# Kernel optimization log

Measured on AMD Instinct MI355X. Metric: run time of the kernel, lower is better.

The kernel has to match this reference:

```python
import jax, jax.numpy as jnp
import numpy as np

N_HEAD = 8
SPAN = 32
BN_EPS = 1e-5


def setup_inputs() -> dict:
    key = jax.random.key(0)
    k1, k2, k3 = jax.random.split(key, 3)
    d_model = 256
    hc = d_model // N_HEAD
    x = jax.random.normal(k1, (4, d_model, 32, 32, 32), dtype=jnp.float32)
    qkv_weight = jax.random.normal(k2, (2 * d_model, d_model), dtype=jnp.float32) * np.sqrt(1.0 / d_model)
    relative = jax.random.normal(k3, (2 * hc, 2 * SPAN - 1), dtype=jnp.float32) * np.sqrt(1.0 / hc)
    gamma = jnp.ones((2 * d_model,), dtype=jnp.float32)
    beta = jnp.zeros((2 * d_model,), dtype=jnp.float32)
    return {"x": x, "qkv_weight": qkv_weight, "relative": relative, "gamma": gamma, "beta": beta}


def _batchnorm1d_train(x, gamma, beta):
    # x: (N, C, L); training-mode BN with batch statistics (biased var)
    mean = x.mean(axis=(0, 2), keepdims=True)
    var = x.var(axis=(0, 2), keepdims=True)
    return (x - mean) * jax.lax.rsqrt(var + BN_EPS) * gamma[None, :, None] + beta[None, :, None]


def reference(x, qkv_weight, relative, gamma, beta):
    B, C, H, W, T = x.shape
    hc = C // N_HEAD
    # width=False: permute (B,C,H,W,T) -> (B,T,W,C,H); attention along H
    xp = jnp.transpose(x, (0, 4, 3, 1, 2)).reshape(B * T * W, C, H)
    # 1x1 conv == channel matmul: (2C,C) x (N,C,H) -> (N,2C,H)
    qkv = jnp.einsum('oc,ncl->nol', qkv_weight, xp)
    qkv = qkv.reshape(B * T * W, N_HEAD, 2 * hc, H)
    q = qkv[:, :, : hc // 2]          # (N, nh, hc/2, H)
    k = qkv[:, :, hc // 2: hc]        # (N, nh, hc/2, H)
    v = qkv[:, :, hc:]                # (N, nh, hc,   H)
    # relative position table gather: all_emb[c,i,j] = relative[c, i+j]
    idx = jnp.arange(SPAN)[:, None] + jnp.arange(SPAN)[None, :]
    all_emb = relative[:, idx]        # (2hc, span, span)
    q_emb = all_emb[: hc // 2]
    k_emb = all_emb[hc // 2: hc]
    v_emb = all_emb[hc:]
    qr = jnp.einsum('nhci,cij->nhij', q, q_emb)
    kr = jnp.einsum('nhci,cij->nhij', k, k_emb)
    qk = jnp.einsum('nhci,nhcj->nhij', q, k)
    sim = jax.nn.softmax(qk + qr + kr, axis=-1)      # (N, nh, H, H)
    sv = jnp.einsum('nhij,nhcj->nhci', sim, v)       # (N, nh, hc, H)
    sve = jnp.einsum('nhij,cij->nhci', sim, v_emb)   # (N, nh, hc, H)
    # cat along last dim then view (N, 2C, H) == interleave sv/sve per (h,c)
    stacked = jnp.stack([sv, sve], axis=3).reshape(B * T * W, 2 * C, H)
    out = _batchnorm1d_train(stacked, gamma, beta)
    out = out.reshape(B, T, W, C, 2, H).sum(axis=4)  # (B,T,W,C,H)
    return jnp.transpose(out, (0, 3, 4, 2, 1))       # (B,C,H,W,T)
```

## Files before the change

kernel.cpp:

```cpp
#include <hip/hip_runtime.h>
#include <hip/hip_bf16.h>


typedef __attribute__((ext_vector_type(8))) short short8;
typedef __attribute__((ext_vector_type(16))) float f32x16;

__device__ inline unsigned short f2bu(float f) {
  __hip_bfloat16 h = __float2bfloat16(f);
  return *(unsigned short*)&h;
}

#define MFMA32(A, B, C) __builtin_amdgcn_mfma_f32_32x32x16_bf16(A, B, C, 0, 0, 0)

constexpr int S_I = 646;
constexpr int S_C = 10;

__global__ __launch_bounds__(256) void k0_wsplit(
    const float* __restrict__ W, unsigned short* __restrict__ Whi,
    unsigned short* __restrict__ Wlo) {
  const int i = blockIdx.x * 256 + threadIdx.x;
  const float w = W[i];
  const unsigned u = __float_as_uint(w);
  const float fhi = __uint_as_float(u & 0xFFFF0000u);
  const float lo = w - fhi;
  Whi[i] = (unsigned short)(u >> 16);
  Wlo[i] = (unsigned short)(__float_as_uint(lo) >> 16);
}

__global__ __launch_bounds__(256) void k1_mfma(
    const unsigned short* __restrict__ Whi, const unsigned short* __restrict__ Wlo,
    const float* __restrict__ x, __hip_bfloat16* __restrict__ qkv) {
  const int td = threadIdx.x, bx = blockIdx.x;
  const int otile = bx & 3, nt = (bx >> 2) & 255, b = bx >> 10;
  const int w = nt & 31, i0 = (nt >> 5) << 2;
  const int o0 = otile * 128;
  const float* xb = x + (size_t)b * 256 * 32768;

  const int wid = td >> 6, l = td & 63, h = l >> 5, n = l & 31;
  const int wo = wid >> 1, wn = wid & 1;

  const int colsp0 = (i0 + (n >> 3)) * 1024 + w * 32 + (wn * 2) * 8 + (n & 7);
  const float* px0 = xb + colsp0 + (size_t)(h * 8) * 32768;
  const float* px1 = px0 + 8;
  const unsigned short* pwh = Whi + (size_t)(o0 + wo * 64 + n) * 256 + h * 8;
  const unsigned short* pwl = Wlo + (size_t)(o0 + wo * 64 + n) * 256 + h * 8;

  const f32x16 zf = {0, 0, 0, 0, 0, 0, 0, 0, 0, 0, 0, 0, 0, 0, 0, 0};
  f32x16 acc[2][2];
#pragma unroll
  for (int it = 0; it < 2; ++it)
#pragma unroll
    for (int jt = 0; jt < 2; ++jt) acc[it][jt] = zf;

#pragma unroll 4
  for (int kf = 0; kf < 16; ++kf) {
    const float* pk0 = px0 + (size_t)kf * 16 * 32768;
    const float* pk1 = px1 + (size_t)kf * 16 * 32768;
    float xv0[8], xv1[8];
#pragma unroll
    for (int e = 0; e < 8; ++e) {
      xv0[e] = pk0[(size_t)e * 32768];
      xv1[e] = pk1[(size_t)e * 32768];
    }
    short8 ahi[2], alo[2];
#pragma unroll
    for (int it = 0; it < 2; ++it) {
      ahi[it] = *(const short8*)(pwh + it * (32 * 256) + kf * 16);
      alo[it] = *(const short8*)(pwl + it * (32 * 256) + kf * 16);
    }
    short8 bhi0, blo0, bhi1, blo1;
#pragma unroll
    for (int e = 0; e < 8; ++e) {
      const unsigned u0 = __float_as_uint(xv0[e]);
      bhi0[e] = (short)(u0 >> 16);
      blo0[e] = (short)(__float_as_uint(xv0[e] - __uint_as_float(u0 & 0xFFFF0000u)) >> 16);
      const unsigned u1 = __float_as_uint(xv1[e]);
      bhi1[e] = (short)(u1 >> 16);
      blo1[e] = (short)(__float_as_uint(xv1[e] - __uint_as_float(u1 & 0xFFFF0000u)) >> 16);
    }
#pragma unroll
    for (int it = 0; it < 2; ++it) {
      acc[it][0] = MFMA32(ahi[it], bhi0, acc[it][0]);
      acc[it][0] = MFMA32(ahi[it], blo0, acc[it][0]);
      acc[it][0] = MFMA32(alo[it], bhi0, acc[it][0]);
      acc[it][1] = MFMA32(ahi[it], bhi1, acc[it][1]);
      acc[it][1] = MFMA32(ahi[it], blo1, acc[it][1]);
      acc[it][1] = MFMA32(alo[it], bhi1, acc[it][1]);
    }
  }

  __hip_bfloat16* qb2 = qkv + ((size_t)((b * 32 + w) * 8 + otile * 2 + wo)) * 65536 +
                        (size_t)(wn * 2) * 16384 + i0 * 8;
#pragma unroll
  for (int jt = 0; jt < 2; ++jt) {
    __hip_bfloat16* bjt = qb2 + jt * 16384;
#pragma unroll
    for (int it = 0; it < 2; ++it) {
#pragma unroll
      for (int r = 0; r < 16; ++r) {
        const int ch = it * 32 + (r & 3) + 8 * (r >> 2) + 4 * h;
        bjt[ch * 256 + n] = __float2bfloat16(acc[it][jt][r]);
      }
    }
  }
}

__global__ __launch_bounds__(256, 3) void k2_attn_mfma(
    const __hip_bfloat16* __restrict__ qkv, const float* __restrict__ rel,
    unsigned int* __restrict__ stk2, float* __restrict__ stats) {
  __shared__ __align__(16) __hip_bfloat16 slab[20672];
  __shared__ __align__(16) unsigned short Sbuf[4 * 1280];
  __shared__ float statb[4][32][4];

  const int bx = blockIdx.x;
  const int w = bx & 31, head = (bx >> 5) & 7, b = bx >> 8;
  const int td = threadIdx.x;
  const int wid = td >> 6, l = td & 63, h = l >> 5, n = l & 31;

  short8 eqf[2], ekf[2], evf[4];
#pragma unroll
  for (int dt = 0; dt < 2; ++dt)
#pragma unroll
    for (int e = 0; e < 8; ++e) {
      int c = h * 8 + e, d = dt * 32 + n;
      eqf[dt][e] = (d < 63) ? (short)f2bu(rel[c * 63 + d]) : (short)0;
      ekf[dt][e] = (d < 63) ? (short)f2bu(rel[(16 + c) * 63 + d]) : (short)0;
    }
#pragma unroll
  for (int kh = 0; kh < 4; ++kh)
#pragma unroll
    for (int e = 0; e < 8; ++e) {
      int d = kh * 16 + h * 8 + e;
      evf[kh][e] = (d < 63) ? (short)f2bu(rel[(32 + n) * 63 + d]) : (short)0;
    }
  short8 ones;
#pragma unroll
  for (int e = 0; e < 8; ++e) ones[e] = (short)0x3F80;

  const __hip_bfloat16* qbase = qkv + ((size_t)((b * 32 + w) * 8 + head)) * 65536;
  unsigned int* sb = stk2 + ((size_t)((b * 8 + head) * 32 + w)) * 32768;
  unsigned short* Sb = Sbuf + wid * 1280;

  const f32x16 zf = {0, 0, 0, 0, 0, 0, 0, 0, 0, 0, 0, 0, 0, 0, 0, 0};
  float st0 = 0, st1 = 0, st2 = 0, st3 = 0;

  for (int tc = 0; tc < 4; ++tc) {
    const int t0 = tc * 8;
    __syncthreads();
    for (int r = 0; r < 8; ++r) {
      int idx = td + 256 * r;
      const uint4 dat = *(const uint4*)(qbase + (size_t)tc * 16384 + (size_t)idx * 8);
      unsigned int* lp = (unsigned int*)(slab + (idx & 31) * S_I + (idx >> 5) * S_C);
      lp[0] = dat.x; lp[1] = dat.y; lp[2] = dat.z; lp[3] = dat.w;
    }
    __syncthreads();
    for (int u = 0; u < 2; ++u) {
      const int tt = 2 * wid + u;
      const int t = t0 + tt;
      short8 aq, ak;
#pragma unroll
      for (int e = 0; e < 8; ++e) {
        aq[e] = *(const short*)&slab[n * S_I + (h * 8 + e) * S_C + tt];
        ak[e] = *(const short*)&slab[n * S_I + (16 + h * 8 + e) * S_C + tt];
      }
      f32x16 qkD = MFMA32(aq, ak, zf);
      f32x16 Rq0 = MFMA32(aq, eqf[0], zf);
      f32x16 Rq1 = MFMA32(aq, eqf[1], zf);
      f32x16 Rk0 = MFMA32(ak, ekf[0], zf);
      f32x16 Rk1 = MFMA32(ak, ekf[1], zf);
#pragma unroll
      for (int r = 0; r < 16; ++r) {
        int rowr = (r & 3) + 8 * (r >> 2) + 4 * h;
        int d = rowr + n;
        int src = (d & 31) + 32 * h;
        float vq0 = __shfl(Rq0[r], src);
        float vq1 = __shfl(Rq1[r], src);
        float vk0 = __shfl(Rk0[r], src);
        float vk1 = __shfl(Rk1[r], src);
        float s = qkD[r] + (d < 32 ? vq0 + vk0 : vq1 + vk1);
        Sb[rowr * 40 + n] = f2bu(__expf(s));
      }
      short8 bv0, bv1;
#pragma unroll
      for (int e = 0; e < 8; ++e) {
        int j0 = h * 8 + e, j1 = 16 + h * 8 + e;
        bv0[e] = *(const short*)&slab[j0 * S_I + (32 + n) * S_C + tt];
        bv1[e] = *(const short*)&slab[j1 * S_I + (32 + n) * S_C + tt];
      }
      short8 as0 = *(const short8*)(Sb + n * 40 + h * 8);
      short8 as1 = *(const short8*)(Sb + n * 40 + 16 + h * 8);
      f32x16 svD = MFMA32(as1, bv1, MFMA32(as0, bv0, zf));
      f32x16 sumD = MFMA32(as1, ones, MFMA32(as0, ones, zf));
      f32x16 sveD = zf;
#pragma unroll
      for (int kh = 0; kh < 4; ++kh) {
        short8 ap;
#pragma unroll
        for (int e = 0; e < 8; ++e) {
          int k = kh * 16 + h * 8 + e;
          int jj = k - n;
          unsigned short raw = Sb[n * 40 + (jj & 31)];
          ap[e] = ((unsigned)jj < 32u) ? (short)raw : (short)0;
        }
        sveD = MFMA32(ap, evf[kh], sveD);
      }
#pragma unroll
      for (int r = 0; r < 16; ++r) {
        int rowr = (r & 3) + 8 * (r >> 2) + 4 * h;
        float inv = 1.0f / sumD[r];
        float svn = svD[r] * inv, sven = sveD[r] * inv;
        st0 += svn; st1 += svn * svn; st2 += sven; st3 += sven * sven;
        unsigned int pk = (unsigned int)f2bu(svn) | ((unsigned int)f2bu(sven) << 16);
        sb[((size_t)rowr * 32 + t) * 32 + n] = pk;
      }
    }
  }
  st0 += __shfl_xor(st0, 32); st1 += __shfl_xor(st1, 32);
  st2 += __shfl_xor(st2, 32); st3 += __shfl_xor(st3, 32);
  if (h == 0) {
    statb[wid][n][0] = st0; statb[wid][n][1] = st1;
    statb[wid][n][2] = st2; statb[wid][n][3] = st3;
  }
  __syncthreads();
  if (td < 32) {
    float a0 = 0, a1 = 0, a2 = 0, a3 = 0;
    for (int wv = 0; wv < 4; ++wv) {
      a0 += statb[wv][td][0]; a1 += statb[wv][td][1];
      a2 += statb[wv][td][2]; a3 += statb[wv][td][3];
    }
    const int o2 = head * 64 + 2 * td;
    atomicAdd(&stats[o2], a0);
    atomicAdd(&stats[o2 + 1], a2);
    atomicAdd(&stats[512 + o2], a1);
    atomicAdd(&stats[512 + o2 + 1], a3);
  }
}

__global__ __launch_bounds__(256) void k3_finalize2(
    const unsigned int* __restrict__ stk2, const float* __restrict__ stats,
    const float* __restrict__ gamma, const float* __restrict__ beta,
    float* __restrict__ out) {
  __shared__ float trans[4][32][33];
  __shared__ float s_sc[64], s_sh[64];
  const int bx = blockIdx.x;
  const int w = bx & 31, head = (bx >> 5) & 7, b = bx >> 8;
  const int td = threadIdx.x;
  if (td < 64) {
    const int o2 = head * 64 + td;
    const float NINV = 1.f / 131072.f;
    float m = stats[o2] * NINV;
    float v = stats[512 + o2] * NINV - m * m;
    float sc = gamma[o2] * rsqrtf(v + 1e-5f);
    s_sc[td] = sc;
    s_sh[td] = beta[o2] - m * sc;
  }
  __syncthreads();
  const unsigned int* pb = stk2 + ((size_t)((b * 8 + head) * 32 + w)) * 32768;
  float* ob = out + ((size_t)(b * 256 + head * 32)) * 32768 + w * 32;
  const int t = td >> 3, c0 = (td & 7) * 4;
  const int t2 = td & 31, cbase = td >> 5;
  for (int i4 = 0; i4 < 32; i4 += 4) {
#pragma unroll
    for (int m = 0; m < 4; ++m) {
      const uint4 dat = *(const uint4*)(pb + (size_t)(i4 + m) * 1024 + td * 4);
      unsigned int dws[4] = {dat.x, dat.y, dat.z, dat.w};
#pragma unroll
      for (int q = 0; q < 4; ++q) {
        int c = c0 + q;
        float sv = __uint_as_float((dws[q] & 0xFFFFu) << 16);
        float sve = __uint_as_float(dws[q] & 0xFFFF0000u);
        trans[m][c][t] =
            sv * s_sc[2 * c] + sve * s_sc[2 * c + 1] + s_sh[2 * c] + s_sh[2 * c + 1];
      }
    }
    __syncthreads();
#pragma unroll
    for (int m = 0; m < 4; ++m) {
#pragma unroll
      for (int cc = 0; cc < 4; ++cc) {
        int c = cbase + 8 * cc;
        ob[(size_t)c * 32768 + (size_t)(i4 + m) * 1024 + t2] = trans[m][c][t2];
      }
    }
    __syncthreads();
  }
}

extern "C" void kernel_launch(void* const* d_in, const int* in_sizes, int n_in,
                              void* d_out, int out_size, void* d_ws, size_t ws_size,
                              hipStream_t stream) {
  const float* x        = (const float*)d_in[0];
  const float* qkv_w    = (const float*)d_in[1];
  const float* relative = (const float*)d_in[2];
  const float* gamma    = (const float*)d_in[3];
  const float* beta     = (const float*)d_in[4];
  float* out = (float*)d_out;

  __hip_bfloat16* qkv = (__hip_bfloat16*)d_ws;
  unsigned int* stk2 = (unsigned int*)((char*)d_ws + (size_t)134217728);
  float* stats = (float*)((char*)d_ws + (size_t)268435456);
  unsigned short* Whi = (unsigned short*)stk2;
  unsigned short* Wlo = Whi + 131072;

  hipMemsetAsync(stats, 0, 1024 * sizeof(float), stream);
  k0_wsplit<<<dim3(512), dim3(256), 0, stream>>>(qkv_w, Whi, Wlo);
  k1_mfma<<<dim3(4096), dim3(256), 0, stream>>>(Whi, Wlo, x, qkv);
  k2_attn_mfma<<<dim3(1024), dim3(256), 0, stream>>>(qkv, relative, stk2, stats);
  k3_finalize2<<<dim3(1024), dim3(256), 0, stream>>>(stk2, stats, gamma, beta, out);
}
```

Before: 693.2 us.

## Pre-split x into transposed bf16 hi/lo buffers instead of splitting weights

A new pre-pass reads x once, splits each value into bf16 hi/lo parts and writes them channel-contiguous per spatial position into workspace. The GEMM kernel then fetches x operands as 16-byte vector loads instead of strided scalar fp32 loads that it converted in-loop, and instead splits the small weight matrix on the fly. The block order is also changed so consecutive blocks share an output tile. This is meant to cut the uncoalesced strided x reads and in-loop conversion work, at the cost of an extra full read/write pass over x (about 128 MB each way) and per-iteration weight conversion.

```diff
diff --git a/kernel.cpp b/kernel.cpp
--- a/kernel.cpp
+++ b/kernel.cpp
@@ -15,91 +15,106 @@
 constexpr int S_I = 646;
 constexpr int S_C = 10;
 
-__global__ __launch_bounds__(256) void k0_wsplit(
-    const float* __restrict__ W, unsigned short* __restrict__ Whi,
-    unsigned short* __restrict__ Wlo) {
-  const int i = blockIdx.x * 256 + threadIdx.x;
-  const float w = W[i];
-  const unsigned u = __float_as_uint(w);
-  const float fhi = __uint_as_float(u & 0xFFFF0000u);
-  const float lo = w - fhi;
-  Whi[i] = (unsigned short)(u >> 16);
-  Wlo[i] = (unsigned short)(__float_as_uint(lo) >> 16);
+__global__ __launch_bounds__(256) void k0_xsplit(
+    const float* __restrict__ x, unsigned short* __restrict__ xThi,
+    unsigned short* __restrict__ xTlo) {
+  const int bx = blockIdx.x;
+  const int spt = bx & 127, kt = (bx >> 7) & 3, b = bx >> 9;
+  const int sp = spt * 256 + threadIdx.x;
+  const int k0 = kt * 64;
+  const float* xs = x + (size_t)b * 8388608 + (size_t)k0 * 32768 + sp;
+  unsigned int hiw[32], low[32];
+#pragma unroll
+  for (int m = 0; m < 32; ++m) {
+    const float f0 = xs[(size_t)(2 * m) * 32768];
+    const float f1 = xs[(size_t)(2 * m + 1) * 32768];
+    const unsigned u0 = __float_as_uint(f0), u1 = __float_as_uint(f1);
+    const float l0 = f0 - __uint_as_float(u0 & 0xFFFF0000u);
+    const float l1 = f1 - __uint_as_float(u1 & 0xFFFF0000u);
+    hiw[m] = (u0 >> 16) | ((u1 >> 16) << 16);
+    low[m] = (__float_as_uint(l0) >> 16) | ((__float_as_uint(l1) >> 16) << 16);
+  }
+  unsigned short* dh = xThi + (size_t)b * 8388608 + (size_t)sp * 256 + k0;
+  unsigned short* dl = xTlo + (size_t)b * 8388608 + (size_t)sp * 256 + k0;
+#pragma unroll
+  for (int q = 0; q < 8; ++q) {
+    uint4 vh, vl;
+    vh.x = hiw[4 * q]; vh.y = hiw[4 * q + 1]; vh.z = hiw[4 * q + 2]; vh.w = hiw[4 * q + 3];
+    vl.x = low[4 * q]; vl.y = low[4 * q + 1]; vl.z = low[4 * q + 2]; vl.w = low[4 * q + 3];
+    *(uint4*)(dh + 8 * q) = vh;
+    *(uint4*)(dl + 8 * q) = vl;
+  }
 }
 
 __global__ __launch_bounds__(256) void k1_mfma(
-    const unsigned short* __restrict__ Whi, const unsigned short* __restrict__ Wlo,
-    const float* __restrict__ x, __hip_bfloat16* __restrict__ qkv) {
+    const float* __restrict__ Wq, const unsigned short* __restrict__ xThi,
+    const unsigned short* __restrict__ xTlo, __hip_bfloat16* __restrict__ qkv) {
   const int td = threadIdx.x, bx = blockIdx.x;
-  const int otile = bx & 3, nt = (bx >> 2) & 255, b = bx >> 10;
+  const int nt = bx & 255, otile = (bx >> 8) & 3, b = bx >> 10;
   const int w = nt & 31, i0 = (nt >> 5) << 2;
   const int o0 = otile * 128;
-  const float* xb = x + (size_t)b * 256 * 32768;
 
   const int wid = td >> 6, l = td & 63, h = l >> 5, n = l & 31;
   const int wo = wid >> 1, wn = wid & 1;
 
-  const int colsp0 = (i0 + (n >> 3)) * 1024 + w * 32 + (wn * 2) * 8 + (n & 7);
-  const float* px0 = xb + colsp0 + (size_t)(h * 8) * 32768;
-  const float* px1 = px0 + 8;
-  const unsigned short* pwh = Whi + (size_t)(o0 + wo * 64 + n) * 256 + h * 8;
-  const unsigned short* pwl = Wlo + (size_t)(o0 + wo * 64 + n) * 256 + h * 8;
+  const int sp0 = (i0 + (n >> 3)) * 1024 + w * 32 + (wn * 2) * 8 + (n & 7);
+  const unsigned short* pxh = xThi + (size_t)b * 8388608 + (size_t)sp0 * 256 + h * 8;
+  const unsigned short* pxl = xTlo + (size_t)b * 8388608 + (size_t)sp0 * 256 + h * 8;
+  const float* pw = Wq + (size_t)(o0 + wo * 64 + n) * 256 + h * 8;
 
   const f32x16 zf = {0, 0, 0, 0, 0, 0, 0, 0, 0, 0, 0, 0, 0, 0, 0, 0};
-  f32x16 acc[2][2];
-#pragma unroll
-  for (int it = 0; it < 2; ++it)
-#pragma unroll
-    for (int jt = 0; jt < 2; ++jt) acc[it][jt] = zf;
-
-#pragma unroll 4
+  f32x16 acc00 = zf, acc01 = zf, acc10 = zf, acc11 = zf;
+
+#pragma unroll 2
   for (int kf = 0; kf < 16; ++kf) {
-    const float* pk0 = px0 + (size_t)kf * 16 * 32768;
-    const float* pk1 = px1 + (size_t)kf * 16 * 32768;
-    float xv0[8], xv1[8];
+    const int kb = kf * 16;
+    const short8 bhi0 = *(const short8*)(pxh + kb);
+    const short8 blo0 = *(const short8*)(pxl + kb);
+    const short8 bhi1 = *(const short8*)(pxh + 2048 + kb);
+    const short8 blo1 = *(const short8*)(pxl + 2048 + kb);
+    const float4 w0a = *(const float4*)(pw + kb);
+    const float4 w0b = *(const float4*)(pw + kb + 4);
+    const float4 w1a = *(const float4*)(pw + 32 * 256 + kb);
+    const float4 w1b = *(const float4*)(pw + 32 * 256 + kb + 4);
+    float wv0[8] = {w0a.x, w0a.y, w0a.z, w0a.w, w0b.x, w0b.y, w0b.z, w0b.w};
+    float wv1[8] = {w1a.x, w1a.y, w1a.z, w1a.w, w1b.x, w1b.y, w1b.z, w1b.w};
+    short8 ahi0, alo0, ahi1, alo1;
 #pragma unroll
     for (int e = 0; e < 8; ++e) {
-      xv0[e] = pk0[(size_t)e * 32768];
-      xv1[e] = pk1[(size_t)e * 32768];
-    }
-    short8 ahi[2], alo[2];
-#pragma unroll
-    for (int it = 0; it < 2; ++it) {
-      ahi[it] = *(const short8*)(pwh + it * (32 * 256) + kf * 16);
-      alo[it] = *(const short8*)(pwl + it * (32 * 256) + kf * 16);
-    }
-    short8 bhi0, blo0, bhi1, blo1;
-#pragma unroll
-    for (int e = 0; e < 8; ++e) {
-      const unsigned u0 = __float_as_uint(xv0[e]);
-      bhi0[e] = (short)(u0 >> 16);
-      blo0[e] = (short)(__float_as_uint(xv0[e] - __uint_as_float(u0 & 0xFFFF0000u)) >> 16);
-      const unsigned u1 = __float_as_uint(xv1[e]);
-      bhi1[e] = (short)(u1 >> 16);
-      blo1[e] = (short)(__float_as_uint(xv1[e] - __uint_as_float(u1 & 0xFFFF0000u)) >> 16);
-    }
-#pragma unroll
-    for (int it = 0; it < 2; ++it) {
-      acc[it][0] = MFMA32(ahi[it], bhi0, acc[it][0]);
-      acc[it][0] = MFMA32(ahi[it], blo0, acc[it][0]);
-      acc[it][0] = MFMA32(alo[it], bhi0, acc[it][0]);
-      acc[it][1] = MFMA32(ahi[it], bhi1, acc[it][1]);
-      acc[it][1] = MFMA32(ahi[it], blo1, acc[it][1]);
-      acc[it][1] = MFMA32(alo[it], bhi1, acc[it][1]);
-    }
+      const unsigned u0 = __float_as_uint(wv0[e]);
+      ahi0[e] = (short)(u0 >> 16);
+      alo0[e] = (short)(__float_as_uint(wv0[e] - __uint_as_float(u0 & 0xFFFF0000u)) >> 16);
+      const unsigned u1 = __float_as_uint(wv1[e]);
+      ahi1[e] = (short)(u1 >> 16);
+      alo1[e] = (short)(__float_as_uint(wv1[e] - __uint_as_float(u1 & 0xFFFF0000u)) >> 16);
+    }
+    acc00 = MFMA32(ahi0, bhi0, acc00);
+    acc00 = MFMA32(ahi0, blo0, acc00);
+    acc00 = MFMA32(alo0, bhi0, acc00);
+    acc01 = MFMA32(ahi0, bhi1, acc01);
+    acc01 = MFMA32(ahi0, blo1, acc01);
+    acc01 = MFMA32(alo0, bhi1, acc01);
+    acc10 = MFMA32(ahi1, bhi0, acc10);
+    acc10 = MFMA32(ahi1, blo0, acc10);
+    acc10 = MFMA32(alo1, bhi0, acc10);
+    acc11 = MFMA32(ahi1, bhi1, acc11);
+    acc11 = MFMA32(ahi1, blo1, acc11);
+    acc11 = MFMA32(alo1, bhi1, acc11);
   }
 
   __hip_bfloat16* qb2 = qkv + ((size_t)((b * 32 + w) * 8 + otile * 2 + wo)) * 65536 +
                         (size_t)(wn * 2) * 16384 + i0 * 8;
+  const f32x16* accs[2][2] = {{&acc00, &acc01}, {&acc10, &acc11}};
 #pragma unroll
   for (int jt = 0; jt < 2; ++jt) {
     __hip_bfloat16* bjt = qb2 + jt * 16384;
 #pragma unroll
     for (int it = 0; it < 2; ++it) {
+      const f32x16 a = *accs[it][jt];
 #pragma unroll
       for (int r = 0; r < 16; ++r) {
         const int ch = it * 32 + (r & 3) + 8 * (r >> 2) + 4 * h;
-        bjt[ch * 256 + n] = __float2bfloat16(acc[it][jt][r]);
+        bjt[ch * 256 + n] = __float2bfloat16(a[r]);
       }
     }
   }
@@ -299,12 +314,12 @@
   __hip_bfloat16* qkv = (__hip_bfloat16*)d_ws;
   unsigned int* stk2 = (unsigned int*)((char*)d_ws + (size_t)134217728);
   float* stats = (float*)((char*)d_ws + (size_t)268435456);
-  unsigned short* Whi = (unsigned short*)stk2;
-  unsigned short* Wlo = Whi + 131072;
+  unsigned short* xThi = (unsigned short*)stk2;
+  unsigned short* xTlo = xThi + 33554432;
 
   hipMemsetAsync(stats, 0, 1024 * sizeof(float), stream);
-  k0_wsplit<<<dim3(512), dim3(256), 0, stream>>>(qkv_w, Whi, Wlo);
-  k1_mfma<<<dim3(4096), dim3(256), 0, stream>>>(Whi, Wlo, x, qkv);
+  k0_xsplit<<<dim3(2048), dim3(256), 0, stream>>>(x, xThi, xTlo);
+  k1_mfma<<<dim3(4096), dim3(256), 0, stream>>>(qkv_w, xThi, xTlo, qkv);
   k2_attn_mfma<<<dim3(1024), dim3(256), 0, stream>>>(qkv, relative, stk2, stats);
   k3_finalize2<<<dim3(1024), dim3(256), 0, stream>>>(stk2, stats, gamma, beta, out);
 }
```

Result: slower. 786.2 us (+13.4%).
